# Optimization experiments

Measured on AMD Instinct MI355X. Metric: run time of the kernel, lower is better.

The kernel has to match this reference:

```python
import jax, jax.numpy as jnp
import numpy as np

B, N, C = 512, 196, 192
HEADS, AGENT = 6, 49
HW = 14  # window side, n = HW*HW


def setup_inputs() -> dict:
    key = jax.random.key(0)
    ks = jax.random.split(key, 16)
    f32 = jnp.float32
    inp = {
        'x': jax.random.normal(ks[0], (B, N, C), f32),
        'qkv_w': jax.random.normal(ks[1], (3 * C, C), f32) * 0.02,
        'qkv_b': jnp.zeros((3 * C,), f32),
        'proj_w': jax.random.normal(ks[2], (C, C), f32) * 0.02,
        'proj_b': jnp.zeros((C,), f32),
        'dwc_w': jax.random.normal(ks[3], (C, 1, 3, 3), f32) * 0.1,
        'dwc_b': jnp.zeros((C,), f32),
        'an_bias': jax.random.normal(ks[4], (HEADS, AGENT, 7, 7), f32) * 0.02,
        'na_bias': jax.random.normal(ks[5], (HEADS, AGENT, 7, 7), f32) * 0.02,
        'ah_bias': jax.random.normal(ks[6], (1, HEADS, AGENT, HW, 1), f32) * 0.02,
        'aw_bias': jax.random.normal(ks[7], (1, HEADS, AGENT, 1, HW), f32) * 0.02,
        'ha_bias': jax.random.normal(ks[8], (1, HEADS, HW, 1, AGENT), f32) * 0.02,
        'wa_bias': jax.random.normal(ks[9], (1, HEADS, 1, HW, AGENT), f32) * 0.02,
    }
    return inp


def reference(x, qkv_w, qkv_b, proj_w, proj_b, dwc_w, dwc_b,
              an_bias, na_bias, ah_bias, aw_bias, ha_bias, wa_bias):
    b, n, c = x.shape
    heads, agent_num = an_bias.shape[0], an_bias.shape[1]
    hd = c // heads
    h = w = int(round(n ** 0.5))
    ps = int(round(agent_num ** 0.5))
    scale = hd ** -0.5

    qkv = x @ qkv_w.T + qkv_b                      # (b, n, 3c)
    q, k, v = jnp.split(qkv, 3, axis=-1)           # each (b, n, c)

    # agent tokens: adaptive avg-pool q spatially to (ps, ps) -- exact stride-r avg pool
    r = h // ps
    agent = q.reshape(b, ps, r, ps, r, c).mean(axis=(2, 4)).reshape(b, agent_num, c)

    qh = q.reshape(b, n, heads, hd).transpose(0, 2, 1, 3)          # (b,h,n,d)
    kh = k.reshape(b, n, heads, hd).transpose(0, 2, 1, 3)
    vh = v.reshape(b, n, heads, hd).transpose(0, 2, 1, 3)
    ag = agent.reshape(b, agent_num, heads, hd).transpose(0, 2, 1, 3)  # (b,h,a,d)

    # stage 1: agent <- kv attention, with interpolated + separable biases
    pb1 = jax.image.resize(an_bias, (heads, agent_num, h, w), method='bilinear')
    pb1 = pb1.reshape(heads, agent_num, n)
    pb2 = (ah_bias + aw_bias).reshape(heads, agent_num, n)
    agent_attn = jax.nn.softmax(
        scale * jnp.einsum('bhad,bhnd->bhan', ag, kh) + pb1 + pb2, axis=-1)
    agent_v = jnp.einsum('bhan,bhnd->bhad', agent_attn, vh)        # (b,h,a,d)

    # stage 2: query <- agent attention
    ab1 = jax.image.resize(na_bias, (heads, agent_num, h, w), method='bilinear')
    ab1 = ab1.reshape(heads, agent_num, n).transpose(0, 2, 1)      # (h,n,a)
    ab2 = (ha_bias + wa_bias).reshape(heads, n, agent_num)
    q_attn = jax.nn.softmax(
        scale * jnp.einsum('bhnd,bhad->bhna', qh, ag) + ab1 + ab2, axis=-1)
    out = jnp.einsum('bhna,bhad->bhnd', q_attn, agent_v)
    out = out.transpose(0, 2, 1, 3).reshape(b, n, c)

    # depthwise-conv residual on v
    v_img = v.reshape(b, h, w, c).transpose(0, 3, 1, 2)            # NCHW
    dw = jax.lax.conv_general_dilated(
        v_img, dwc_w, (1, 1), ((1, 1), (1, 1)),
        dimension_numbers=('NCHW', 'OIHW', 'NCHW'), feature_group_count=c)
    dw = dw + dwc_b[None, :, None, None]
    out = out + dw.transpose(0, 2, 3, 1).reshape(b, n, c)

    return out @ proj_w.T + proj_b
```

## Files before the change

kernel.cpp:

```cpp
#include <hip/hip_runtime.h>
#include <hip/hip_fp16.h>

typedef unsigned short u16;
typedef __bf16 bf16x8 __attribute__((ext_vector_type(8)));
typedef float f32x4 __attribute__((ext_vector_type(4)));

#define SCALE 0.17677669529663687f
#define LOG2E 1.4426950408889634f
#define SCALE2 (0.17677669529663687f * 1.4426950408889634f)

__device__ __forceinline__ float bf2f(u16 u) {
  union { unsigned int i; float f; } x; x.i = ((unsigned int)u) << 16; return x.f;
}
__device__ __forceinline__ u16 f2bf(float f) {
  union { __bf16 h; u16 u; } x; x.h = (__bf16)f; return x.u;
}
__device__ __forceinline__ u16 f2h(float f) {
  union { __half h; u16 u; } x; x.h = __float2half(f); return x.u;
}
__device__ __forceinline__ float fexp2(float x) {
#if __has_builtin(__builtin_amdgcn_exp2f)
  return __builtin_amdgcn_exp2f(x);
#else
  return exp2f(x);
#endif
}
__device__ __forceinline__ uint4 pack8(const u16* h) {
  uint4 r;
  r.x = (unsigned)h[0] | ((unsigned)h[1] << 16);
  r.y = (unsigned)h[2] | ((unsigned)h[3] << 16);
  r.z = (unsigned)h[4] | ((unsigned)h[5] << 16);
  r.w = (unsigned)h[6] | ((unsigned)h[7] << 16);
  return r;
}
__device__ __forceinline__ uint2 pk4(float a, float b, float c, float d) {
  uint2 r;
  r.x = (unsigned)f2bf(a) | ((unsigned)f2bf(b) << 16);
  r.y = (unsigned)f2bf(c) | ((unsigned)f2bf(d) << 16);
  return r;
}
__device__ __forceinline__ bf16x8 zfrag() {
  bf16x8 z;
  #pragma unroll
  for (int j = 0; j < 8; ++j) z[j] = (__bf16)0.0f;
  return z;
}
__device__ __forceinline__ uint2 shfl_u2(uint2 v, int src) {
  uint2 r;
  r.x = (unsigned)__shfl((int)v.x, src);
  r.y = (unsigned)__shfl((int)v.y, src);
  return r;
}

#define LSTR 72
#define ASTR 200

__global__ __launch_bounds__(256) void k_qkv(
    const float* __restrict__ Ag, const u16* __restrict__ Wq, const float* __restrict__ biasg,
    u16* __restrict__ qo, u16* __restrict__ ko, u16* __restrict__ vo)
{
  __shared__ __align__(16) u16 As[64 * ASTR];
  __shared__ __align__(16) u16 Bs[64 * ASTR];
  const int og = blockIdx.x / 1568, mt = blockIdx.x % 1568;
  const int tid = threadIdx.x, lane = tid & 63, wid = tid >> 6;
  const int wt = wid >> 1, wc = wid & 1;
  const int lm = lane & 15, kg = lane >> 4;

  #pragma unroll
  for (int i = 0; i < 6; ++i) {
    int c = tid + i * 256;
    int row = c / 24, cc = (c % 24) * 8;
    const float* s = Ag + (size_t)(mt * 64 + row) * 192 + cc;
    float f[8];
    *(float4*)f = *(const float4*)s;
    *(float4*)(f + 4) = *(const float4*)(s + 4);
    u16 h[8];
    #pragma unroll
    for (int j = 0; j < 8; ++j) h[j] = f2bf(f[j]);
    *(uint4*)(As + row * ASTR + cc) = pack8(h);
  }

  u16* const dst = (og == 0) ? qo : (og == 1) ? ko : vo;

  for (int nt = 0; nt < 3; ++nt) {
    __syncthreads();
    #pragma unroll
    for (int i = 0; i < 6; ++i) {
      int c = tid + i * 256;
      int row = c / 24, cc = (c % 24) * 8;
      *(uint4*)(Bs + row * ASTR + cc) =
          *(const uint4*)(Wq + (size_t)(og * 192 + nt * 64 + row) * 192 + cc);
    }
    __syncthreads();

    f32x4 acc[2][2] = {};
    #pragma unroll
    for (int ks = 0; ks < 6; ++ks) {
      bf16x8 xfr[2];
      #pragma unroll
      for (int tf = 0; tf < 2; ++tf)
        xfr[tf] = *(const bf16x8*)(As + (wt * 32 + tf * 16 + lm) * ASTR + ks * 32 + kg * 8);
      #pragma unroll
      for (int cf = 0; cf < 2; ++cf) {
        bf16x8 wfr = *(const bf16x8*)(Bs + (wc * 32 + cf * 16 + lm) * ASTR + ks * 32 + kg * 8);
        #pragma unroll
        for (int tf = 0; tf < 2; ++tf)
          acc[cf][tf] = __builtin_amdgcn_mfma_f32_16x16x32_bf16(wfr, xfr[tf], acc[cf][tf], 0, 0, 0);
      }
    }

    #pragma unroll
    for (int cf = 0; cf < 2; ++cf) {
      int cc = nt * 64 + wc * 32 + cf * 16 + kg * 4;
      int hh = cc >> 5, dd = cc & 31;
      f32x4 bv = *(const f32x4*)(biasg + og * 192 + cc);
      #pragma unroll
      for (int tf = 0; tf < 2; ++tf) {
        int tg = mt * 64 + wt * 32 + tf * 16 + lm;
        int bq = tg / 196, tok = tg - bq * 196;
        *(uint2*)(dst + (((size_t)bq * 6 + hh) * 196 + tok) * 32 + dd) =
            pk4(acc[cf][tf][0] + bv[0], acc[cf][tf][1] + bv[1],
                acc[cf][tf][2] + bv[2], acc[cf][tf][3] + bv[3]);
      }
    }
  }
}

__global__ __launch_bounds__(256) void k_proj(
    const u16* __restrict__ Ag, const u16* __restrict__ Wh, const u16* __restrict__ Wl,
    const float* __restrict__ biasg, float* __restrict__ og)
{
  __shared__ __align__(16) u16 As[128 * LSTR];
  __shared__ __align__(16) u16 Bh[64 * LSTR];
  __shared__ __align__(16) u16 Bl[64 * LSTR];
  const int mt = blockIdx.x / 3, nt = blockIdx.x % 3;
  const int tid = threadIdx.x, lane = tid & 63, wid = tid >> 6;
  const int wm = wid >> 1, wn = wid & 1;
  const int lm = lane & 15, kg = lane >> 4;

  f32x4 acc[4][2] = {};
  const int aoffbase = (wm * 64 + lm) * LSTR + kg * 8;
  const int boffbase = (wn * 32 + lm) * LSTR + kg * 8;

  for (int kt = 0; kt < 3; ++kt) {
    #pragma unroll
    for (int i = 0; i < 4; ++i) {
      int c = tid + i * 256;
      int row = c >> 3, cc = (c & 7) * 8;
      *(uint4*)(As + row * LSTR + cc) =
          *(const uint4*)(Ag + (size_t)(mt * 128 + row) * 192 + kt * 64 + cc);
    }
    #pragma unroll
    for (int i = 0; i < 2; ++i) {
      int c = tid + i * 256;
      int row = c >> 3, cc = (c & 7) * 8;
      size_t src = (size_t)(nt * 64 + row) * 192 + kt * 64 + cc;
      *(uint4*)(Bh + row * LSTR + cc) = *(const uint4*)(Wh + src);
      *(uint4*)(Bl + row * LSTR + cc) = *(const uint4*)(Wl + src);
    }
    __syncthreads();
    #pragma unroll
    for (int ks = 0; ks < 2; ++ks) {
      bf16x8 bh_[2], bl_[2];
      #pragma unroll
      for (int nf = 0; nf < 2; ++nf) {
        bh_[nf] = *(const bf16x8*)(Bh + boffbase + nf * 16 * LSTR + ks * 32);
        bl_[nf] = *(const bf16x8*)(Bl + boffbase + nf * 16 * LSTR + ks * 32);
      }
      #pragma unroll
      for (int mf = 0; mf < 4; ++mf) {
        bf16x8 af = *(const bf16x8*)(As + aoffbase + mf * 16 * LSTR + ks * 32);
        #pragma unroll
        for (int nf = 0; nf < 2; ++nf) {
          acc[mf][nf] = __builtin_amdgcn_mfma_f32_16x16x32_bf16(af, bh_[nf], acc[mf][nf], 0, 0, 0);
          acc[mf][nf] = __builtin_amdgcn_mfma_f32_16x16x32_bf16(af, bl_[nf], acc[mf][nf], 0, 0, 0);
        }
      }
    }
    __syncthreads();
  }

  #pragma unroll
  for (int mf = 0; mf < 4; ++mf) {
    int m0 = mt * 128 + wm * 64 + mf * 16 + kg * 4;
    #pragma unroll
    for (int nf = 0; nf < 2; ++nf) {
      int col = nt * 64 + wn * 32 + nf * 16 + lm;
      float bias = biasg[col];
      #pragma unroll
      for (int r = 0; r < 4; ++r)
        og[(size_t)(m0 + r) * 192 + col] = acc[mf][nf][r] + bias;
    }
  }
}

__global__ __launch_bounds__(256) void k_pool(const u16* __restrict__ qg, u16* __restrict__ agg)
{
  int idx = blockIdx.x * 256 + threadIdx.x;
  int d8 = idx & 3;
  int a = (idx >> 2) % 49;
  int bh = idx / (49 * 4);
  int py = a / 7, px = a - py * 7;
  int n0 = (py * 2) * 14 + px * 2;
  const u16* qb = qg + (size_t)bh * 196 * 32 + d8 * 8;
  uint4 r0 = *(const uint4*)(qb + n0 * 32);
  uint4 r1 = *(const uint4*)(qb + (n0 + 1) * 32);
  uint4 r2 = *(const uint4*)(qb + (n0 + 14) * 32);
  uint4 r3 = *(const uint4*)(qb + (n0 + 15) * 32);
  const u16 *p0 = (const u16*)&r0, *p1 = (const u16*)&r1, *p2 = (const u16*)&r2, *p3 = (const u16*)&r3;
  u16 o[8];
  #pragma unroll
  for (int j = 0; j < 8; ++j)
    o[j] = f2bf(0.25f * (bf2f(p0[j]) + bf2f(p1[j]) + bf2f(p2[j]) + bf2f(p3[j])));
  *(uint4*)(agg + (size_t)idx * 8) = pack8(o);
}

__device__ __forceinline__ void lerpw(int i, int& j0, int& j1, float& f) {
  float xx = 0.5f * i - 0.25f;
  int j = (int)floorf(xx);
  f = xx - j;
  if (j < 0) { j = 0; f = 0.f; }
  j0 = j;
  j1 = (j + 1 > 6) ? 6 : j + 1;
}
__device__ __forceinline__ float bilin7(const float* src, int y, int x) {
  int y0, y1, x0, x1; float fy, fx;
  lerpw(y, y0, y1, fy); lerpw(x, x0, x1, fx);
  float v00 = src[y0 * 7 + x0], v01 = src[y0 * 7 + x1];
  float v10 = src[y1 * 7 + x0], v11 = src[y1 * 7 + x1];
  return (1.f - fy) * ((1.f - fx) * v00 + fx * v01) + fy * ((1.f - fx) * v10 + fx * v11);
}
__global__ __launch_bounds__(256) void k_bias(
    const float* __restrict__ an_, const float* __restrict__ na_,
    const float* __restrict__ ah_, const float* __restrict__ aw_,
    const float* __restrict__ ha_, const float* __restrict__ wa_,
    const float* __restrict__ qw_, const float* __restrict__ pw_,
    float* __restrict__ b1, float* __restrict__ b2, u16* __restrict__ wq,
    u16* __restrict__ wph, u16* __restrict__ wpl)
{
  int i = blockIdx.x * 256 + threadIdx.x;
  const int T1 = 6 * 49 * 208;
  const int T2 = 6 * 196 * 64;
  const int T3 = 576 * 192;
  const int T4 = 192 * 192;
  if (i < T1) {
    int n = i % 208, a = (i / 208) % 49, h = i / (208 * 49);
    float v = 0.f;
    if (n < 196) {
      int y = n / 14, x = n - y * 14;
      v = bilin7(an_ + (h * 49 + a) * 49, y, x)
        + ah_[(h * 49 + a) * 14 + y] + aw_[(h * 49 + a) * 14 + x];
    }
    b1[i] = v * LOG2E;
  } else if (i < T1 + T2) {
    int j = i - T1;
    int a = j & 63, n = (j >> 6) % 196, h = j / (196 * 64);
    float v = 0.f;
    if (a < 49) {
      int y = n / 14, x = n - y * 14;
      v = bilin7(na_ + (h * 49 + a) * 49, y, x)
        + ha_[(h * 14 + y) * 49 + a] + wa_[(h * 14 + x) * 49 + a];
    }
    b2[j] = v * LOG2E;
  } else if (i < T1 + T2 + T3) {
    int j = i - T1 - T2;
    wq[j] = f2bf(qw_[j]);
  } else if (i < T1 + T2 + T3 + T4) {
    int j = i - T1 - T2 - T3;
    float w = pw_[j];
    u16 hi = f2bf(w);
    wph[j] = hi;
    wpl[j] = f2bf(w - bf2f(hi));
  }
}

#define PSTR 216
#define QSTR 72
#define VSTR 40

__global__ __launch_bounds__(256, 4) void k_attn(
    const u16* __restrict__ qg, const u16* __restrict__ kgl, const u16* __restrict__ vgl,
    const u16* __restrict__ agg, const float* __restrict__ b1p, const float* __restrict__ b2p,
    const float* __restrict__ dwcw, const float* __restrict__ dwcb,
    u16* __restrict__ preg)
{
  __shared__ __align__(16) u16 vt[32 * PSTR];
  __shared__ __align__(16) u16 vrm[196 * VSTR];
  __shared__ __align__(16) u16 avt[32 * QSTR];
  __shared__ __align__(16) float wdl[320];

  const int bh = blockIdx.x, h = bh % 6, b = bh / 6;
  const int tid = threadIdx.x, lane = tid & 63, w = tid >> 6;
  const int lm = lane & 15, kg = lane >> 4;
  const size_t base = (size_t)bh * (196 * 32);

  for (int c = tid; c < 784; c += 256) {
    int row = c >> 2, d0 = (c & 3) * 8;
    uint4 vv = *(const uint4*)(vgl + base + row * 32 + d0);
    const u16* pv = (const u16*)&vv;
    u16 hf[8];
    #pragma unroll
    for (int j = 0; j < 8; ++j) {
      vt[(d0 + j) * PSTR + row] = pv[j];
      hf[j] = f2h(bf2f(pv[j]));
    }
    *(uint4*)(vrm + row * VSTR + d0) = pack8(hf);
  }
  for (int c = tid; c < 192; c += 256) {
    int row = c / 6, col = 98 + c % 6;
    ((unsigned*)vt)[row * (PSTR / 2) + col] = 0;
  }
  for (int c = tid; c < 320; c += 256) {
    if (c < 288) {
      int tap = c >> 5, d = c & 31;
      wdl[tap * 32 + d] = dwcw[h * 288 + d * 9 + tap];
    } else {
      wdl[c] = dwcb[h * 32 + (c - 288)];
    }
  }

  const size_t agbase = (size_t)bh * 49 * 32;
  bf16x8 agw;
  {
    int a = 16 * w + lm;
    agw = (a < 49) ? *(const bf16x8*)(agg + agbase + a * 32 + kg * 8) : zfrag();
  }

  f32x4 acc1[13];
  #pragma unroll
  for (int t = 0; t < 13; ++t) {
    bf16x8 afr = *(const bf16x8*)(kgl + base + (16 * t + lm) * 32 + kg * 8);
    acc1[t] = __builtin_amdgcn_mfma_f32_16x16x32_bf16(afr, agw, (f32x4){0.f, 0.f, 0.f, 0.f}, 0, 0, 0);
  }

  const int arow = 16 * w + lm;
  uint2 p1pk[13];
  float inv1;
  {
    const float* b1base = b1p + ((size_t)(h * 49 + arow) * 208 + 4 * kg);
    #pragma unroll
    for (int t = 0; t < 13; ++t) {
      f32x4 bv = (arow < 49) ? *(const f32x4*)(b1base + 16 * t) : (f32x4){0.f, 0.f, 0.f, 0.f};
      #pragma unroll
      for (int r = 0; r < 4; ++r) acc1[t][r] = acc1[t][r] * SCALE2 + bv[r];
    }
    float sum = 0.f;
    #pragma unroll
    for (int t = 0; t < 13; ++t) {
      #pragma unroll
      for (int r = 0; r < 4; ++r) {
        float e = (t < 12 || kg == 0) ? fexp2(acc1[t][r]) : 0.f;
        acc1[t][r] = e; sum += e;
      }
    }
    sum += __shfl_xor(sum, 16);
    sum += __shfl_xor(sum, 32);
    inv1 = 1.0f / sum;
    #pragma unroll
    for (int t = 0; t < 13; ++t)
      p1pk[t] = pk4(acc1[t][0], acc1[t][1], acc1[t][2], acc1[t][3]);
  }

  __syncthreads();

  f32x4 accav[2] = {{0.f, 0.f, 0.f, 0.f}, {0.f, 0.f, 0.f, 0.f}};
  const int sl = (lane & 15) | (((2 * kg) & 3) << 4);
  const int sh = (lane & 15) | (((2 * kg + 1) & 3) << 4);
  #pragma unroll
  for (int kt = 0; kt < 6; ++kt) {
    uint2 e0 = shfl_u2(p1pk[2 * kt], sl);
    uint2 e1 = shfl_u2(p1pk[2 * kt + 1], sl);
    uint2 o0 = shfl_u2(p1pk[2 * kt], sh);
    uint2 o1 = shfl_u2(p1pk[2 * kt + 1], sh);
    uint2 lo = (kg & 2) ? e1 : e0;
    uint2 hi = (kg & 2) ? o1 : o0;
    union { uint4 u; bf16x8 v; } a_;
    a_.u = make_uint4(lo.x, lo.y, hi.x, hi.y);
    #pragma unroll
    for (int nt = 0; nt < 2; ++nt) {
      bf16x8 bfr = *(const bf16x8*)(vt + (16 * nt + lm) * PSTR + kt * 32 + kg * 8);
      accav[nt] = __builtin_amdgcn_mfma_f32_16x16x32_bf16(a_.v, bfr, accav[nt], 0, 0, 0);
    }
  }
  {
    union { uint4 u; bf16x8 v; } a_;
    a_.u = make_uint4(p1pk[12].x, p1pk[12].y, 0u, 0u);
    #pragma unroll
    for (int nt = 0; nt < 2; ++nt) {
      uint2 vv = *(const uint2*)(vt + (16 * nt + lm) * PSTR + 192 + kg * 4);
      union { uint4 u; bf16x8 v; } b_;
      b_.u = make_uint4(vv.x, vv.y, 0u, 0u);
      accav[nt] = __builtin_amdgcn_mfma_f32_16x16x32_bf16(a_.v, b_.v, accav[nt], 0, 0, 0);
    }
  }

  float si[4];
  #pragma unroll
  for (int r = 0; r < 4; ++r) si[r] = __shfl(inv1, kg * 4 + r);

  #pragma unroll
  for (int nt = 0; nt < 2; ++nt)
    *(uint2*)(avt + (16 * nt + lm) * QSTR + 16 * w + 4 * kg) =
        pk4(accav[nt][0] * si[0], accav[nt][1] * si[1],
            accav[nt][2] * si[2], accav[nt][3] * si[3]);

  bf16x8 qf[4];
  #pragma unroll
  for (int i = 0; i < 4; ++i) {
    int nt = w + 4 * i;
    int row = 16 * nt + lm;
    if (nt < 13 && row < 196)
      qf[i] = *(const bf16x8*)(qg + base + row * 32 + kg * 8);
    else
      qf[i] = zfrag();
  }
  bf16x8 agf[4];
  #pragma unroll
  for (int mt = 0; mt < 4; ++mt) {
    int a = 16 * mt + lm;
    if (a < 49) agf[mt] = *(const bf16x8*)(agg + agbase + a * 32 + kg * 8);
    else agf[mt] = zfrag();
  }

  __syncthreads();

  #pragma unroll
  for (int i = 0; i < 4; ++i) {
    int nt = w + 4 * i;
    if (nt < 13) {
      const int ncol = 16 * nt + lm;
      f32x4 acc2[4];
      #pragma unroll
      for (int mt = 0; mt < 4; ++mt)
        acc2[mt] = __builtin_amdgcn_mfma_f32_16x16x32_bf16(agf[mt], qf[i], (f32x4){0.f, 0.f, 0.f, 0.f}, 0, 0, 0);
      const float* b2base = b2p + ((size_t)(h * 196 + (ncol < 196 ? ncol : 0)) * 64 + 4 * kg);
      #pragma unroll
      for (int mt = 0; mt < 4; ++mt) {
        f32x4 bv = (ncol < 196) ? *(const f32x4*)(b2base + 16 * mt) : (f32x4){0.f, 0.f, 0.f, 0.f};
        #pragma unroll
        for (int r = 0; r < 4; ++r) acc2[mt][r] = acc2[mt][r] * SCALE2 + bv[r];
      }
      float sum = 0.f;
      #pragma unroll
      for (int mt = 0; mt < 4; ++mt) {
        #pragma unroll
        for (int r = 0; r < 4; ++r) {
          bool valid = (mt < 3) || (kg == 0 && r == 0);
          float e = valid ? fexp2(acc2[mt][r]) : 0.f;
          acc2[mt][r] = e; sum += e;
        }
      }
      sum += __shfl_xor(sum, 16);
      sum += __shfl_xor(sum, 32);
      const float inv = 1.0f / sum;
      uint2 p2pk[4];
      #pragma unroll
      for (int mt = 0; mt < 4; ++mt)
        p2pk[mt] = pk4(acc2[mt][0], acc2[mt][1], acc2[mt][2], acc2[mt][3]);

      f32x4 acc4[2] = {{0.f, 0.f, 0.f, 0.f}, {0.f, 0.f, 0.f, 0.f}};
      #pragma unroll
      for (int kt = 0; kt < 2; ++kt) {
        uint2 e0 = shfl_u2(p2pk[2 * kt], sl);
        uint2 e1 = shfl_u2(p2pk[2 * kt + 1], sl);
        uint2 o0 = shfl_u2(p2pk[2 * kt], sh);
        uint2 o1 = shfl_u2(p2pk[2 * kt + 1], sh);
        uint2 lo = (kg & 2) ? e1 : e0;
        uint2 hi = (kg & 2) ? o1 : o0;
        union { uint4 u; bf16x8 v; } b_;
        b_.u = make_uint4(lo.x, lo.y, hi.x, hi.y);
        #pragma unroll
        for (int mt2 = 0; mt2 < 2; ++mt2) {
          bf16x8 afr = *(const bf16x8*)(avt + (16 * mt2 + lm) * QSTR + kt * 32 + kg * 8);
          acc4[mt2] = __builtin_amdgcn_mfma_f32_16x16x32_bf16(afr, b_.v, acc4[mt2], 0, 0, 0);
        }
      }
      if (ncol < 196) {
        const int y = ncol / 14, x = ncol - y * 14;
        float dw[2][4];
        #pragma unroll
        for (int mt = 0; mt < 2; ++mt) {
          f32x4 bv = *(const f32x4*)(wdl + 288 + 16 * mt + 4 * kg);
          #pragma unroll
          for (int r = 0; r < 4; ++r) dw[mt][r] = bv[r];
        }
        #pragma unroll
        for (int ky = 0; ky < 3; ++ky) {
          int yy = y + ky - 1;
          if (yy < 0 || yy > 13) continue;
          #pragma unroll
          for (int kx = 0; kx < 3; ++kx) {
            int xx = x + kx - 1;
            if (xx < 0 || xx > 13) continue;
            int nv = yy * 14 + xx;
            int tap = ky * 3 + kx;
            #pragma unroll
            for (int mt = 0; mt < 2; ++mt) {
              f32x4 wv = *(const f32x4*)(wdl + tap * 32 + 16 * mt + 4 * kg);
              const __half2* hv = (const __half2*)(vrm + nv * VSTR + 16 * mt + 4 * kg);
              __half2 h0 = hv[0], h1 = hv[1];
              dw[mt][0] += wv[0] * __low2float(h0);
              dw[mt][1] += wv[1] * __high2float(h0);
              dw[mt][2] += wv[2] * __low2float(h1);
              dw[mt][3] += wv[3] * __high2float(h1);
            }
          }
        }
        u16* orow = preg + ((size_t)b * 196 + ncol) * 192 + h * 32;
        #pragma unroll
        for (int mt = 0; mt < 2; ++mt)
          *(uint2*)(orow + 16 * mt + 4 * kg) =
              pk4(acc4[mt][0] * inv + dw[mt][0], acc4[mt][1] * inv + dw[mt][1],
                  acc4[mt][2] * inv + dw[mt][2], acc4[mt][3] * inv + dw[mt][3]);
      }
    }
  }
}

extern "C" void kernel_launch(void* const* d_in, const int* in_sizes, int n_in,
                              void* d_out, int out_size, void* d_ws, size_t ws_size,
                              hipStream_t stream)
{
  (void)in_sizes; (void)n_in; (void)out_size;
  const float* x      = (const float*)d_in[0];
  const float* qkv_w  = (const float*)d_in[1];
  const float* qkv_b  = (const float*)d_in[2];
  const float* proj_w = (const float*)d_in[3];
  const float* proj_b = (const float*)d_in[4];
  const float* dwc_w  = (const float*)d_in[5];
  const float* dwc_b  = (const float*)d_in[6];
  const float* an_b   = (const float*)d_in[7];
  const float* na_b   = (const float*)d_in[8];
  const float* ah_b   = (const float*)d_in[9];
  const float* aw_b   = (const float*)d_in[10];
  const float* ha_b   = (const float*)d_in[11];
  const float* wa_b   = (const float*)d_in[12];

  const size_t SZ_QKV = (size_t)512 * 6 * 196 * 32 * 2;
  const size_t SZ_AG  = (size_t)512 * 6 * 49 * 32 * 2;
  const size_t SZ_B1  = (((size_t)6 * 49 * 208 * 4) + 255) & ~(size_t)255;
  const size_t SZ_B2  = (size_t)6 * 196 * 64 * 4;
  const size_t SZ_WQ  = (((size_t)576 * 192 * 2) + 255) & ~(size_t)255;
  const size_t SZ_WP  = (((size_t)192 * 192 * 2) + 255) & ~(size_t)255;

  char* ws = (char*)d_ws;
  u16*   qb    = (u16*)(ws);
  u16*   kb    = (u16*)(ws + SZ_QKV);
  u16*   vb    = (u16*)(ws + 2 * SZ_QKV);
  u16*   agb   = (u16*)(ws + 3 * SZ_QKV);
  float* b1    = (float*)(ws + 3 * SZ_QKV + SZ_AG);
  float* b2    = (float*)(ws + 3 * SZ_QKV + SZ_AG + SZ_B1);
  u16*   preb  = (u16*)(ws + 3 * SZ_QKV + SZ_AG + SZ_B1 + SZ_B2);
  u16*   wqb   = (u16*)(ws + 3 * SZ_QKV + SZ_AG + SZ_B1 + SZ_B2 + SZ_QKV);
  u16*   wph   = (u16*)(ws + 3 * SZ_QKV + SZ_AG + SZ_B1 + SZ_B2 + SZ_QKV + SZ_WQ);
  u16*   wpl   = (u16*)(ws + 3 * SZ_QKV + SZ_AG + SZ_B1 + SZ_B2 + SZ_QKV + SZ_WQ + SZ_WP);

  const size_t need = 3 * SZ_QKV + SZ_AG + SZ_B1 + SZ_B2 + SZ_QKV + SZ_WQ + 2 * SZ_WP;
  if (ws_size < need) return;

  const int TOT = 6 * 49 * 208 + 6 * 196 * 64 + 576 * 192 + 192 * 192;
  k_bias<<<(TOT + 255) / 256, 256, 0, stream>>>(an_b, na_b, ah_b, aw_b, ha_b, wa_b,
                                                qkv_w, proj_w, b1, b2, wqb, wph, wpl);
  k_qkv<<<1568 * 3, 256, 0, stream>>>(x, wqb, qkv_b, qb, kb, vb);
  k_pool<<<2352, 256, 0, stream>>>(qb, agb);
  k_attn<<<3072, 256, 0, stream>>>(qb, kb, vb, agb, b1, b2, dwc_w, dwc_b, preb);
  k_proj<<<784 * 3, 256, 0, stream>>>(preb, wph, wpl, proj_b, (float*)d_out);
}
```

Measured before the change: 173.2 us.

## Compute all QKV outputs per x tile and pad transposed V smem rows

```diff
diff --git a/kernel.cpp b/kernel.cpp
--- a/kernel.cpp
+++ b/kernel.cpp
@@ -55,20 +55,20 @@
 #define LSTR 72
 #define ASTR 200
 
-__global__ __launch_bounds__(256) void k_qkv(
+__global__ __launch_bounds__(512) void k_qkv(
     const float* __restrict__ Ag, const u16* __restrict__ Wq, const float* __restrict__ biasg,
     u16* __restrict__ qo, u16* __restrict__ ko, u16* __restrict__ vo)
 {
   __shared__ __align__(16) u16 As[64 * ASTR];
   __shared__ __align__(16) u16 Bs[64 * ASTR];
-  const int og = blockIdx.x / 1568, mt = blockIdx.x % 1568;
+  const int mt = blockIdx.x;
   const int tid = threadIdx.x, lane = tid & 63, wid = tid >> 6;
-  const int wt = wid >> 1, wc = wid & 1;
+  const int wt = wid >> 2, wc = wid & 3;
   const int lm = lane & 15, kg = lane >> 4;
 
   #pragma unroll
-  for (int i = 0; i < 6; ++i) {
-    int c = tid + i * 256;
+  for (int i = 0; i < 3; ++i) {
+    int c = tid + i * 512;
     int row = c / 24, cc = (c % 24) * 8;
     const float* s = Ag + (size_t)(mt * 64 + row) * 192 + cc;
     float f[8];
@@ -80,48 +80,40 @@
     *(uint4*)(As + row * ASTR + cc) = pack8(h);
   }
 
-  u16* const dst = (og == 0) ? qo : (og == 1) ? ko : vo;
-
-  for (int nt = 0; nt < 3; ++nt) {
+  for (int nt = 0; nt < 9; ++nt) {
     __syncthreads();
     #pragma unroll
-    for (int i = 0; i < 6; ++i) {
-      int c = tid + i * 256;
+    for (int i = 0; i < 3; ++i) {
+      int c = tid + i * 512;
       int row = c / 24, cc = (c % 24) * 8;
       *(uint4*)(Bs + row * ASTR + cc) =
-          *(const uint4*)(Wq + (size_t)(og * 192 + nt * 64 + row) * 192 + cc);
+          *(const uint4*)(Wq + (size_t)(nt * 64 + row) * 192 + cc);
     }
     __syncthreads();
 
-    f32x4 acc[2][2] = {};
+    f32x4 acc[2] = {};
     #pragma unroll
     for (int ks = 0; ks < 6; ++ks) {
-      bf16x8 xfr[2];
-      #pragma unroll
-      for (int tf = 0; tf < 2; ++tf)
-        xfr[tf] = *(const bf16x8*)(As + (wt * 32 + tf * 16 + lm) * ASTR + ks * 32 + kg * 8);
-      #pragma unroll
-      for (int cf = 0; cf < 2; ++cf) {
-        bf16x8 wfr = *(const bf16x8*)(Bs + (wc * 32 + cf * 16 + lm) * ASTR + ks * 32 + kg * 8);
-        #pragma unroll
-        for (int tf = 0; tf < 2; ++tf)
-          acc[cf][tf] = __builtin_amdgcn_mfma_f32_16x16x32_bf16(wfr, xfr[tf], acc[cf][tf], 0, 0, 0);
-      }
-    }
-
-    #pragma unroll
-    for (int cf = 0; cf < 2; ++cf) {
-      int cc = nt * 64 + wc * 32 + cf * 16 + kg * 4;
-      int hh = cc >> 5, dd = cc & 31;
-      f32x4 bv = *(const f32x4*)(biasg + og * 192 + cc);
+      bf16x8 wfr = *(const bf16x8*)(Bs + (wc * 16 + lm) * ASTR + ks * 32 + kg * 8);
       #pragma unroll
       for (int tf = 0; tf < 2; ++tf) {
-        int tg = mt * 64 + wt * 32 + tf * 16 + lm;
-        int bq = tg / 196, tok = tg - bq * 196;
-        *(uint2*)(dst + (((size_t)bq * 6 + hh) * 196 + tok) * 32 + dd) =
-            pk4(acc[cf][tf][0] + bv[0], acc[cf][tf][1] + bv[1],
-                acc[cf][tf][2] + bv[2], acc[cf][tf][3] + bv[3]);
-      }
+        bf16x8 xfr = *(const bf16x8*)(As + (wt * 32 + tf * 16 + lm) * ASTR + ks * 32 + kg * 8);
+        acc[tf] = __builtin_amdgcn_mfma_f32_16x16x32_bf16(wfr, xfr, acc[tf], 0, 0, 0);
+      }
+    }
+
+    int col = nt * 64 + wc * 16 + kg * 4;
+    int which = col / 192, cc2 = col - which * 192;
+    int hh = cc2 >> 5, dd = cc2 & 31;
+    f32x4 bv = *(const f32x4*)(biasg + col);
+    u16* dst = (which == 0) ? qo : (which == 1) ? ko : vo;
+    #pragma unroll
+    for (int tf = 0; tf < 2; ++tf) {
+      int tg = mt * 64 + wt * 32 + tf * 16 + lm;
+      int bq = tg / 196, tok = tg - bq * 196;
+      *(uint2*)(dst + (((size_t)bq * 6 + hh) * 196 + tok) * 32 + dd) =
+          pk4(acc[tf][0] + bv[0], acc[tf][1] + bv[1],
+              acc[tf][2] + bv[2], acc[tf][3] + bv[3]);
     }
   }
 }
@@ -274,7 +266,7 @@
   }
 }
 
-#define PSTR 216
+#define VTSTR 264
 #define QSTR 72
 #define VSTR 40
 
@@ -284,7 +276,7 @@
     const float* __restrict__ dwcw, const float* __restrict__ dwcb,
     u16* __restrict__ preg)
 {
-  __shared__ __align__(16) u16 vt[32 * PSTR];
+  __shared__ __align__(16) u16 vt[32 * VTSTR];
   __shared__ __align__(16) u16 vrm[196 * VSTR];
   __shared__ __align__(16) u16 avt[32 * QSTR];
   __shared__ __align__(16) float wdl[320];
@@ -299,16 +291,17 @@
     uint4 vv = *(const uint4*)(vgl + base + row * 32 + d0);
     const u16* pv = (const u16*)&vv;
     u16 hf[8];
+    int tb = d0 * VTSTR + (d0 >> 3) * 16 + row;
     #pragma unroll
     for (int j = 0; j < 8; ++j) {
-      vt[(d0 + j) * PSTR + row] = pv[j];
+      vt[tb + j * VTSTR] = pv[j];
       hf[j] = f2h(bf2f(pv[j]));
     }
     *(uint4*)(vrm + row * VSTR + d0) = pack8(hf);
   }
-  for (int c = tid; c < 192; c += 256) {
-    int row = c / 6, col = 98 + c % 6;
-    ((unsigned*)vt)[row * (PSTR / 2) + col] = 0;
+  for (int c = tid; c < 384; c += 256) {
+    int d = c / 12, n = 196 + c % 12;
+    vt[d * VTSTR + (d >> 3) * 16 + n] = 0;
   }
   for (int c = tid; c < 320; c += 256) {
     if (c < 288) {
@@ -378,7 +371,8 @@
     a_.u = make_uint4(lo.x, lo.y, hi.x, hi.y);
     #pragma unroll
     for (int nt = 0; nt < 2; ++nt) {
-      bf16x8 bfr = *(const bf16x8*)(vt + (16 * nt + lm) * PSTR + kt * 32 + kg * 8);
+      const int vd = 16 * nt + lm;
+      bf16x8 bfr = *(const bf16x8*)(vt + vd * VTSTR + (vd >> 3) * 16 + kt * 32 + kg * 8);
       accav[nt] = __builtin_amdgcn_mfma_f32_16x16x32_bf16(a_.v, bfr, accav[nt], 0, 0, 0);
     }
   }
@@ -387,7 +381,8 @@
     a_.u = make_uint4(p1pk[12].x, p1pk[12].y, 0u, 0u);
     #pragma unroll
     for (int nt = 0; nt < 2; ++nt) {
-      uint2 vv = *(const uint2*)(vt + (16 * nt + lm) * PSTR + 192 + kg * 4);
+      const int vd = 16 * nt + lm;
+      uint2 vv = *(const uint2*)(vt + vd * VTSTR + (vd >> 3) * 16 + 192 + 4 * kg);
       union { uint4 u; bf16x8 v; } b_;
       b_.u = make_uint4(vv.x, vv.y, 0u, 0u);
       accav[nt] = __builtin_amdgcn_mfma_f32_16x16x32_bf16(a_.v, b_.v, accav[nt], 0, 0, 0);
@@ -561,7 +556,7 @@
   const int TOT = 6 * 49 * 208 + 6 * 196 * 64 + 576 * 192 + 192 * 192;
   k_bias<<<(TOT + 255) / 256, 256, 0, stream>>>(an_b, na_b, ah_b, aw_b, ha_b, wa_b,
                                                 qkv_w, proj_w, b1, b2, wqb, wph, wpl);
-  k_qkv<<<1568 * 3, 256, 0, stream>>>(x, wqb, qkv_b, qb, kb, vb);
+  k_qkv<<<1568, 512, 0, stream>>>(x, wqb, qkv_b, qb, kb, vb);
   k_pool<<<2352, 256, 0, stream>>>(qb, agb);
   k_attn<<<3072, 256, 0, stream>>>(qb, kb, vb, agb, b1, b2, dwc_w, dwc_b, preb);
   k_proj<<<784 * 3, 256, 0, stream>>>(preb, wph, wpl, proj_b, (float*)d_out);
```

New measurement: 176.8 us. +2.1%, slower.
